# Performance work log

Measured on AMD Instinct MI355X. Metric: run time of the kernel, lower is better.

Reference implementation:

```python
import jax, jax.numpy as jnp
import numpy as np

HEADS = 12
HEAD_SIZE = 64
HIDDEN = 768


def _rope_tables(seqlen, dim, dtype):
    inv_freq = 1.0 / (10000.0 ** (jnp.arange(0, dim, 2, dtype=jnp.float32) / dim))
    t = jnp.arange(seqlen, dtype=jnp.float32)
    freqs = t[:, None] * inv_freq[None, :]  # [L, dim/2]
    return jnp.sin(freqs).astype(dtype), jnp.cos(freqs).astype(dtype)


def _apply_rope(x, sin, cos):
    # x: [B, L, H, D]; sin/cos: [L, D/2] -> broadcast as [1, L, 1, D/2]
    sin = sin[None, :, None, :]
    cos = cos[None, :, None, :]
    x1 = x[..., 0::2]
    x2 = x[..., 1::2]
    out1 = x1 * cos - x2 * sin
    out2 = x1 * sin + x2 * cos
    # interleave back: stack on new last axis then flatten
    return jnp.stack([out1, out2], axis=-1).reshape(x.shape)


def setup_inputs() -> dict:
    key = jax.random.key(0)
    k1, k2, k3 = jax.random.split(key, 3)
    B, L = 8, 512
    inputs = jax.random.normal(k1, (B, L, HIDDEN), dtype=jnp.float32)
    attention_mask = jnp.ones((B, L), dtype=jnp.int32)
    out_dim = HEADS * 2 * HEAD_SIZE
    W = jax.random.normal(k2, (HIDDEN, out_dim), dtype=jnp.float32) * (1.0 / np.sqrt(HIDDEN))
    b = jax.random.normal(k3, (out_dim,), dtype=jnp.float32) * 0.02
    return {"inputs": inputs, "W": W, "b": b, "attention_mask": attention_mask}


def reference(inputs, W, b, attention_mask):
    B, L, _ = inputs.shape
    x = inputs @ W + b  # [B, L, H*2*D]
    x = x.reshape(B, L, HEADS, 2, HEAD_SIZE)
    qw = x[..., 0, :]  # [B, L, H, D]
    kw = x[..., 1, :]
    sin, cos = _rope_tables(L, HEAD_SIZE, x.dtype)
    qw = _apply_rope(qw, sin, cos)
    kw = _apply_rope(kw, sin, cos)
    logits = jnp.einsum('bmhd,bnhd->bhmn', qw, kw) / np.sqrt(HEAD_SIZE)
    neg_inf = jnp.finfo(logits.dtype).min
    am = attention_mask.astype(bool)
    valid = am[:, None, None, :] & am[:, None, :, None]
    logits = jnp.where(valid, logits, neg_inf)
    tri = jnp.tril(jnp.ones((L, L), dtype=bool), k=-1)
    logits = jnp.where(tri[None, None, :, :], neg_inf, logits)
    return logits
```

## Files before the change

### kernel.cpp

```cpp
#include <hip/hip_runtime.h>
#include <hip/hip_bf16.h>
#include <math.h>
#include <stdint.h>

constexpr int BATCH  = 8;
constexpr int SEQ    = 512;
constexpr int HEADS  = 12;
constexpr int HSIZE  = 64;
constexpr int HIDDEN = 768;
constexpr int OUTD   = 1536;
constexpr int M      = BATCH * SEQ;
constexpr int BH     = BATCH * HEADS;

#define NEG_INF (-3.3895313892515355e38f)

typedef short  s16x8 __attribute__((ext_vector_type(8)));
typedef float  f32x4 __attribute__((ext_vector_type(4)));

__device__ __forceinline__ short f2bf(float f) {
    __hip_bfloat16 h = __float2bfloat16(f);
    return *reinterpret_cast<short*>(&h);
}

__device__ __forceinline__ void g2l16(const void* g, void* l) {
    __builtin_amdgcn_global_load_lds(
        reinterpret_cast<const __attribute__((address_space(1))) int*>(
            reinterpret_cast<uintptr_t>(g)),
        reinterpret_cast<__attribute__((address_space(3))) int*>(
            reinterpret_cast<uintptr_t>(l)),
        16, 0, 0);
}

__global__ __launch_bounds__(256) void prep_kernel(
    const float* __restrict__ X,  short* __restrict__ Xb,
    const float* __restrict__ W,  short* __restrict__ Wt,
    float* __restrict__ sc_sin,   float* __restrict__ sc_cos)
{
    __shared__ short Ls[32][36];
    const int b   = blockIdx.x;
    const int tid = threadIdx.x;

    if (b < 1536) {
        const int t = b * 256 + tid;
        const float4 a = ((const float4*)X)[t * 2];
        const float4 c = ((const float4*)X)[t * 2 + 1];
        s16x8 o;
        o[0] = f2bf(a.x); o[1] = f2bf(a.y); o[2] = f2bf(a.z); o[3] = f2bf(a.w);
        o[4] = f2bf(c.x); o[5] = f2bf(c.y); o[6] = f2bf(c.z); o[7] = f2bf(c.w);
        ((s16x8*)Xb)[t] = o;
    } else if (b < 2688) {
        const int bid = b - 1536;
        const int nx = bid % 48, ky = bid / 48;
        const int r  = tid >> 3;
        const int c4 = (tid & 7) * 4;
        const float4 v = *(const float4*)(W + (size_t)(ky * 32 + r) * OUTD + nx * 32 + c4);
        Ls[r][c4 + 0] = f2bf(v.x); Ls[r][c4 + 1] = f2bf(v.y);
        Ls[r][c4 + 2] = f2bf(v.z); Ls[r][c4 + 3] = f2bf(v.w);
        __syncthreads();
        short4 ov;
        ov.x = Ls[c4 + 0][r]; ov.y = Ls[c4 + 1][r];
        ov.z = Ls[c4 + 2][r]; ov.w = Ls[c4 + 3][r];
        *(short4*)(Wt + (size_t)(nx * 32 + r) * HIDDEN + ky * 32 + c4) = ov;
    } else {
        const int t   = (b - 2688) * 256 + tid;
        const int pos = t >> 5, pi = t & 31;
        const float invf = exp2f((float)(2 * pi) * (-13.287712379549449f / 64.0f));
        const float ang  = (float)pos * invf;
        sc_sin[t] = sinf(ang);
        sc_cos[t] = cosf(ang);
    }
}

__global__ __launch_bounds__(256) void proj_mfma_kernel(
    const short* __restrict__ Xb,
    const short* __restrict__ Wt,
    const float* __restrict__ bias,
    const float* __restrict__ sc_sin,
    const float* __restrict__ sc_cos,
    short* __restrict__ Qb,
    short* __restrict__ Kb)
{
    union Sh {
        struct { short As[2][128 * 64]; short Bs[2][64 * 64]; } st;
        float epi[128 * 68];
    };
    __shared__ Sh sh;

    const int tid = threadIdx.x;
    const int l   = tid & 63;
    const int w   = tid >> 6;
    const int mBase = blockIdx.y * 128;
    const int nBase = blockIdx.x * 64;
    const int wm = w * 32;

    const int lr = l >> 3;
    const int gc = (l & 7) ^ lr;
    const short* aSrc = Xb + (size_t)(mBase + wm + lr)     * HIDDEN + gc * 8;
    const short* bSrc = Wt + (size_t)(nBase + w * 16 + lr) * HIDDEN + gc * 8;

#define STAGE(buf_, k0_)                                                     \
    do {                                                                     \
        _Pragma("unroll")                                                    \
        for (int p = 0; p < 4; ++p)                                          \
            g2l16(aSrc + (k0_) + p * 8 * HIDDEN,                             \
                  sh.st.As[buf_] + (w * 4 + p) * 512);                       \
        _Pragma("unroll")                                                    \
        for (int p = 0; p < 2; ++p)                                          \
            g2l16(bSrc + (k0_) + p * 8 * HIDDEN,                             \
                  sh.st.Bs[buf_] + (w * 2 + p) * 512);                       \
    } while (0)

    STAGE(0, 0);
    __syncthreads();

    f32x4 acc[2][4] = {};
    int buf = 0;

    for (int k0 = 0; k0 < HIDDEN; k0 += 64) {
        if (k0 + 64 < HIDDEN)
            STAGE(buf ^ 1, k0 + 64);
        const short* Asb = sh.st.As[buf];
        const short* Bsb = sh.st.Bs[buf];
#pragma unroll
        for (int s = 0; s < 2; ++s) {
            const int c = ((s * 4 + (l >> 4)) ^ (l & 7)) * 8;
            s16x8 af[2], bf[4];
#pragma unroll
            for (int i = 0; i < 2; ++i)
                af[i] = *(const s16x8*)(Asb + (wm + i * 16 + (l & 15)) * 64 + c);
#pragma unroll
            for (int j = 0; j < 4; ++j)
                bf[j] = *(const s16x8*)(Bsb + (j * 16 + (l & 15)) * 64 + c);
#pragma unroll
            for (int i = 0; i < 2; ++i)
#pragma unroll
                for (int j = 0; j < 4; ++j)
                    acc[i][j] = __builtin_amdgcn_mfma_f32_16x16x32_bf16(
                        af[i], bf[j], acc[i][j], 0, 0, 0);
        }
        __syncthreads();
        buf ^= 1;
    }
#undef STAGE

    const int colL = l & 15, quad = l >> 4;
#pragma unroll
    for (int j = 0; j < 4; ++j) {
        const int nl = j * 16 + colL;
#pragma unroll
        for (int i = 0; i < 2; ++i)
#pragma unroll
            for (int r = 0; r < 4; ++r)
                sh.epi[(wm + i * 16 + quad * 4 + r) * 68 + nl] = acc[i][j][r];
    }
    __syncthreads();

    const int bb   = mBase >> 9;
    const int pos0 = mBase & 511;
    const int h    = nBase >> 7;
    const int slot = (nBase >> 6) & 1;
    short* dst = (slot ? Kb : Qb) + ((size_t)(bb * HEADS + h) * SEQ + pos0) * HSIZE;

#pragma unroll
    for (int p = 0; p < 4; ++p) {
        const int c    = tid + p * 256;
        const int mrow = c >> 3;
        const int ch   = c & 7;
        const int dloc = ch * 8;
        const int pos  = pos0 + mrow;

        const float* src = &sh.epi[mrow * 68 + dloc];
        const float4 v0 = *(const float4*)(src);
        const float4 v1 = *(const float4*)(src + 4);
        const float* bp = bias + nBase + dloc;
        const float4 b0 = *(const float4*)(bp);
        const float4 b1 = *(const float4*)(bp + 4);
        const float4 sn = *(const float4*)(sc_sin + pos * 32 + (dloc >> 1));
        const float4 cs = *(const float4*)(sc_cos + pos * 32 + (dloc >> 1));

        const float e0 = v0.x + b0.x, o0 = v0.y + b0.y;
        const float e1 = v0.z + b0.z, o1 = v0.w + b0.w;
        const float e2 = v1.x + b1.x, o2 = v1.y + b1.y;
        const float e3 = v1.z + b1.z, o3 = v1.w + b1.w;
        s16x8 ov;
        ov[0] = f2bf(e0 * cs.x - o0 * sn.x); ov[1] = f2bf(e0 * sn.x + o0 * cs.x);
        ov[2] = f2bf(e1 * cs.y - o1 * sn.y); ov[3] = f2bf(e1 * sn.y + o1 * cs.y);
        ov[4] = f2bf(e2 * cs.z - o2 * sn.z); ov[5] = f2bf(e2 * sn.z + o2 * cs.z);
        ov[6] = f2bf(e3 * cs.w - o3 * sn.w); ov[7] = f2bf(e3 * sn.w + o3 * cs.w);
        *(s16x8*)(dst + (size_t)mrow * HSIZE + dloc) = ov;
    }
}

__global__ __launch_bounds__(256) void qk_mfma_kernel(
    const short* __restrict__ Qb,
    const short* __restrict__ Kb,
    const int*   __restrict__ am,
    float* __restrict__ out)
{
    const int bh = blockIdx.z;
    const int bb = bh / HEADS;
    const int m0 = blockIdx.y * 128;
    const int n0 = blockIdx.x * 128;
    const int tid = threadIdx.x;

    if (m0 >= n0 + 128) {
        const float4 ninf = make_float4(NEG_INF, NEG_INF, NEG_INF, NEG_INF);
        float* base = out + ((size_t)bh * SEQ + m0) * SEQ + n0;
        const int c = (tid & 31) * 4;
#pragma unroll
        for (int r = 0; r < 16; ++r) {
            const int row = r * 8 + (tid >> 5);
            *(float4*)(base + (size_t)row * SEQ + c) = ninf;
        }
        return;
    }

    __shared__ short Qs[128 * 64];
    __shared__ short Ks[128 * 64];
    __shared__ __align__(16) int amR[128];
    __shared__ __align__(16) int amC[128];

    const int l = tid & 63;
    const int w = tid >> 6;
    if (tid < 128)      amR[tid]       = am[bb * SEQ + m0 + tid];
    else                amC[tid - 128] = am[bb * SEQ + n0 + (tid - 128)];

    const int lr = l >> 3;
    const int gc = (l & 7) ^ lr;
    const short* qSrc = Qb + ((size_t)bh * SEQ + m0 + w * 32 + lr) * HSIZE + gc * 8;
    const short* kSrc = Kb + ((size_t)bh * SEQ + n0 + w * 32 + lr) * HSIZE + gc * 8;
#pragma unroll
    for (int p = 0; p < 4; ++p) {
        g2l16(qSrc + p * 8 * HSIZE, Qs + (w * 4 + p) * 512);
        g2l16(kSrc + p * 8 * HSIZE, Ks + (w * 4 + p) * 512);
    }
    __syncthreads();

    const int wm = (w & 1) * 64;
    const int wn = (w >> 1) * 64;
    f32x4 acc[4][4] = {};
#pragma unroll
    for (int s = 0; s < 2; ++s) {
        const int c = ((s * 4 + (l >> 4)) ^ (l & 7)) * 8;
        s16x8 qf[4], kf[4];
#pragma unroll
        for (int i = 0; i < 4; ++i) {
            qf[i] = *(const s16x8*)(Qs + (wm + i * 16 + (l & 15)) * 64 + c);
            kf[i] = *(const s16x8*)(Ks + (wn + i * 16 + (l & 15)) * 64 + c);
        }
#pragma unroll
        for (int i = 0; i < 4; ++i)
#pragma unroll
            for (int j = 0; j < 4; ++j)
                acc[i][j] = __builtin_amdgcn_mfma_f32_16x16x32_bf16(
                    qf[i], kf[j], acc[i][j], 0, 0, 0);
    }

    const int colL = l & 15, quad = l >> 4;
    int rm[4][4];
#pragma unroll
    for (int i = 0; i < 4; ++i)
#pragma unroll
        for (int r = 0; r < 4; ++r)
            rm[i][r] = amR[wm + i * 16 + quad * 4 + r];

#pragma unroll
    for (int j = 0; j < 4; ++j) {
        const int nl = wn + j * 16 + colL;
        const int ng = n0 + nl;
        const int an = amC[nl];
#pragma unroll
        for (int i = 0; i < 4; ++i) {
#pragma unroll
            for (int r = 0; r < 4; ++r) {
                const int ml = wm + i * 16 + quad * 4 + r;
                const int mg = m0 + ml;
                float v = acc[i][j][r] * 0.125f;
                if (ng < mg || !an || !rm[i][r]) v = NEG_INF;
                out[((size_t)bh * SEQ + mg) * SEQ + ng] = v;
            }
        }
    }
}

extern "C" void kernel_launch(void* const* d_in, const int* in_sizes, int n_in,
                              void* d_out, int out_size, void* d_ws, size_t ws_size,
                              hipStream_t stream) {
    const float* X    = (const float*)d_in[0];
    const float* W    = (const float*)d_in[1];
    const float* bias = (const float*)d_in[2];
    const int*   am   = (const int*)d_in[3];
    float* out = (float*)d_out;

    char* ws = (char*)d_ws;
    short* Xb = (short*)(ws);
    short* Wt = (short*)(ws + 6291456);
    short* Qb = (short*)(ws + 8650752);
    short* Kb = (short*)(ws + 14942208);
    float* sc_sin = (float*)(ws + 21233664);
    float* sc_cos = (float*)(ws + 21299200);

    prep_kernel<<<dim3(2752), 256, 0, stream>>>(X, Xb, W, Wt, sc_sin, sc_cos);
    proj_mfma_kernel<<<dim3(OUTD / 64, M / 128), 256, 0, stream>>>(
        Xb, Wt, bias, sc_sin, sc_cos, Qb, Kb);
    qk_mfma_kernel<<<dim3(SEQ / 128, SEQ / 128, BH), 256, 0, stream>>>(Qb, Kb, am, out);
}
```

Baseline: 144.3 us.

## Fuse prep, projection and QK kernels into one cooperative persistent kernel

Merges the three launches into a single cooperative kernel of 768 blocks. Grid-wide syncs separate the bf16 conversion and RoPE table phase, the projection GEMM phase and the QK logits phase. The aim is to remove launch overhead and inter-kernel gaps. In exchange it adds two grid barriers, limits occupancy to a fixed grid (launch_bounds 256,3), and grid-strides the prep and QK phases, so each block does about two QK tiles serially.

```diff
diff --git a/kernel.cpp b/kernel.cpp
--- a/kernel.cpp
+++ b/kernel.cpp
@@ -1,7 +1,10 @@
 #include <hip/hip_runtime.h>
+#include <hip/hip_cooperative_groups.h>
 #include <hip/hip_bf16.h>
 #include <math.h>
 #include <stdint.h>
+
+namespace cg = cooperative_groups;
 
 constexpr int BATCH  = 8;
 constexpr int SEQ    = 512;
@@ -31,253 +34,247 @@
         16, 0, 0);
 }
 
-__global__ __launch_bounds__(256) void prep_kernel(
-    const float* __restrict__ X,  short* __restrict__ Xb,
-    const float* __restrict__ W,  short* __restrict__ Wt,
-    float* __restrict__ sc_sin,   float* __restrict__ sc_cos)
+__global__ __launch_bounds__(256, 3) void fused_kernel(
+    const float* __restrict__ X,      short* __restrict__ Xb,
+    const float* __restrict__ W,      short* __restrict__ Wt,
+    const float* __restrict__ bias,
+    float* __restrict__ sc_sin,       float* __restrict__ sc_cos,
+    short* __restrict__ Qb,           short* __restrict__ Kb,
+    const int* __restrict__ am,       float* __restrict__ out)
 {
-    __shared__ short Ls[32][36];
-    const int b   = blockIdx.x;
-    const int tid = threadIdx.x;
-
-    if (b < 1536) {
-        const int t = b * 256 + tid;
-        const float4 a = ((const float4*)X)[t * 2];
-        const float4 c = ((const float4*)X)[t * 2 + 1];
-        s16x8 o;
-        o[0] = f2bf(a.x); o[1] = f2bf(a.y); o[2] = f2bf(a.z); o[3] = f2bf(a.w);
-        o[4] = f2bf(c.x); o[5] = f2bf(c.y); o[6] = f2bf(c.z); o[7] = f2bf(c.w);
-        ((s16x8*)Xb)[t] = o;
-    } else if (b < 2688) {
-        const int bid = b - 1536;
-        const int nx = bid % 48, ky = bid / 48;
-        const int r  = tid >> 3;
-        const int c4 = (tid & 7) * 4;
-        const float4 v = *(const float4*)(W + (size_t)(ky * 32 + r) * OUTD + nx * 32 + c4);
-        Ls[r][c4 + 0] = f2bf(v.x); Ls[r][c4 + 1] = f2bf(v.y);
-        Ls[r][c4 + 2] = f2bf(v.z); Ls[r][c4 + 3] = f2bf(v.w);
-        __syncthreads();
-        short4 ov;
-        ov.x = Ls[c4 + 0][r]; ov.y = Ls[c4 + 1][r];
-        ov.z = Ls[c4 + 2][r]; ov.w = Ls[c4 + 3][r];
-        *(short4*)(Wt + (size_t)(nx * 32 + r) * HIDDEN + ky * 32 + c4) = ov;
-    } else {
-        const int t   = (b - 2688) * 256 + tid;
-        const int pos = t >> 5, pi = t & 31;
-        const float invf = exp2f((float)(2 * pi) * (-13.287712379549449f / 64.0f));
-        const float ang  = (float)pos * invf;
-        sc_sin[t] = sinf(ang);
-        sc_cos[t] = cosf(ang);
-    }
-}
-
-__global__ __launch_bounds__(256) void proj_mfma_kernel(
-    const short* __restrict__ Xb,
-    const short* __restrict__ Wt,
-    const float* __restrict__ bias,
-    const float* __restrict__ sc_sin,
-    const float* __restrict__ sc_cos,
-    short* __restrict__ Qb,
-    short* __restrict__ Kb)
-{
-    union Sh {
-        struct { short As[2][128 * 64]; short Bs[2][64 * 64]; } st;
-        float epi[128 * 68];
-    };
-    __shared__ Sh sh;
+    __shared__ __align__(16) union {
+        short Ls[32][36];
+        union {
+            struct { short As[2][128 * 64]; short Bs[2][64 * 64]; } st;
+            float epi[128 * 68];
+        } proj;
+        struct { short Qs[128 * 64]; short Ks[128 * 64];
+                 int amR[128]; int amC[128]; } qk;
+    } sh;
 
     const int tid = threadIdx.x;
     const int l   = tid & 63;
     const int w   = tid >> 6;
-    const int mBase = blockIdx.y * 128;
-    const int nBase = blockIdx.x * 64;
-    const int wm = w * 32;
-
-    const int lr = l >> 3;
-    const int gc = (l & 7) ^ lr;
-    const short* aSrc = Xb + (size_t)(mBase + wm + lr)     * HIDDEN + gc * 8;
-    const short* bSrc = Wt + (size_t)(nBase + w * 16 + lr) * HIDDEN + gc * 8;
+
+    for (int vb = blockIdx.x; vb < 2752; vb += 768) {
+        __syncthreads();
+        if (vb < 1536) {
+            const int t = vb * 256 + tid;
+            const float4 a = ((const float4*)X)[t * 2];
+            const float4 c = ((const float4*)X)[t * 2 + 1];
+            s16x8 o;
+            o[0] = f2bf(a.x); o[1] = f2bf(a.y); o[2] = f2bf(a.z); o[3] = f2bf(a.w);
+            o[4] = f2bf(c.x); o[5] = f2bf(c.y); o[6] = f2bf(c.z); o[7] = f2bf(c.w);
+            ((s16x8*)Xb)[t] = o;
+        } else if (vb < 2688) {
+            const int bid = vb - 1536;
+            const int nx = bid % 48, ky = bid / 48;
+            const int r  = tid >> 3;
+            const int c4 = (tid & 7) * 4;
+            const float4 v = *(const float4*)(W + (size_t)(ky * 32 + r) * OUTD + nx * 32 + c4);
+            sh.Ls[r][c4 + 0] = f2bf(v.x); sh.Ls[r][c4 + 1] = f2bf(v.y);
+            sh.Ls[r][c4 + 2] = f2bf(v.z); sh.Ls[r][c4 + 3] = f2bf(v.w);
+            __syncthreads();
+            short4 ov;
+            ov.x = sh.Ls[c4 + 0][r]; ov.y = sh.Ls[c4 + 1][r];
+            ov.z = sh.Ls[c4 + 2][r]; ov.w = sh.Ls[c4 + 3][r];
+            *(short4*)(Wt + (size_t)(nx * 32 + r) * HIDDEN + ky * 32 + c4) = ov;
+        } else {
+            const int t   = (vb - 2688) * 256 + tid;
+            const int pos = t >> 5, pi = t & 31;
+            const float invf = exp2f((float)(2 * pi) * (-13.287712379549449f / 64.0f));
+            const float ang  = (float)pos * invf;
+            sc_sin[t] = sinf(ang);
+            sc_cos[t] = cosf(ang);
+        }
+    }
+
+    __threadfence();
+    cg::this_grid().sync();
+
+    {
+        const int mBase = (blockIdx.x / 24) * 128;
+        const int nBase = (blockIdx.x % 24) * 64;
+        const int wm = w * 32;
+
+        const int lr = l >> 3;
+        const int gc = (l & 7) ^ lr;
+        const short* aSrc = Xb + (size_t)(mBase + wm + lr)     * HIDDEN + gc * 8;
+        const short* bSrc = Wt + (size_t)(nBase + w * 16 + lr) * HIDDEN + gc * 8;
 
 #define STAGE(buf_, k0_)                                                     \
     do {                                                                     \
         _Pragma("unroll")                                                    \
         for (int p = 0; p < 4; ++p)                                          \
             g2l16(aSrc + (k0_) + p * 8 * HIDDEN,                             \
-                  sh.st.As[buf_] + (w * 4 + p) * 512);                       \
+                  sh.proj.st.As[buf_] + (w * 4 + p) * 512);                  \
         _Pragma("unroll")                                                    \
         for (int p = 0; p < 2; ++p)                                          \
             g2l16(bSrc + (k0_) + p * 8 * HIDDEN,                             \
-                  sh.st.Bs[buf_] + (w * 2 + p) * 512);                       \
+                  sh.proj.st.Bs[buf_] + (w * 2 + p) * 512);                  \
     } while (0)
 
-    STAGE(0, 0);
-    __syncthreads();
-
-    f32x4 acc[2][4] = {};
-    int buf = 0;
-
-    for (int k0 = 0; k0 < HIDDEN; k0 += 64) {
-        if (k0 + 64 < HIDDEN)
-            STAGE(buf ^ 1, k0 + 64);
-        const short* Asb = sh.st.As[buf];
-        const short* Bsb = sh.st.Bs[buf];
+        STAGE(0, 0);
+        __syncthreads();
+
+        f32x4 acc[2][4] = {};
+        int buf = 0;
+
+        for (int k0 = 0; k0 < HIDDEN; k0 += 64) {
+            if (k0 + 64 < HIDDEN)
+                STAGE(buf ^ 1, k0 + 64);
+            const short* Asb = sh.proj.st.As[buf];
+            const short* Bsb = sh.proj.st.Bs[buf];
+#pragma unroll
+            for (int s = 0; s < 2; ++s) {
+                const int c = ((s * 4 + (l >> 4)) ^ (l & 7)) * 8;
+                s16x8 af[2], bf[4];
+#pragma unroll
+                for (int i = 0; i < 2; ++i)
+                    af[i] = *(const s16x8*)(Asb + (wm + i * 16 + (l & 15)) * 64 + c);
+#pragma unroll
+                for (int j = 0; j < 4; ++j)
+                    bf[j] = *(const s16x8*)(Bsb + (j * 16 + (l & 15)) * 64 + c);
+#pragma unroll
+                for (int i = 0; i < 2; ++i)
+#pragma unroll
+                    for (int j = 0; j < 4; ++j)
+                        acc[i][j] = __builtin_amdgcn_mfma_f32_16x16x32_bf16(
+                            af[i], bf[j], acc[i][j], 0, 0, 0);
+            }
+            __syncthreads();
+            buf ^= 1;
+        }
+#undef STAGE
+
+        const int colL = l & 15, quad = l >> 4;
+#pragma unroll
+        for (int j = 0; j < 4; ++j) {
+            const int nl = j * 16 + colL;
+#pragma unroll
+            for (int i = 0; i < 2; ++i)
+#pragma unroll
+                for (int r = 0; r < 4; ++r)
+                    sh.proj.epi[(wm + i * 16 + quad * 4 + r) * 68 + nl] = acc[i][j][r];
+        }
+        __syncthreads();
+
+        const int bb   = mBase >> 9;
+        const int pos0 = mBase & 511;
+        const int h    = nBase >> 7;
+        const int slot = (nBase >> 6) & 1;
+        short* dst = (slot ? Kb : Qb) + ((size_t)(bb * HEADS + h) * SEQ + pos0) * HSIZE;
+
+#pragma unroll
+        for (int p = 0; p < 4; ++p) {
+            const int c    = tid + p * 256;
+            const int mrow = c >> 3;
+            const int ch   = c & 7;
+            const int dloc = ch * 8;
+            const int pos  = pos0 + mrow;
+
+            const float* src = &sh.proj.epi[mrow * 68 + dloc];
+            const float4 v0 = *(const float4*)(src);
+            const float4 v1 = *(const float4*)(src + 4);
+            const float* bp = bias + nBase + dloc;
+            const float4 b0 = *(const float4*)(bp);
+            const float4 b1 = *(const float4*)(bp + 4);
+            const float4 sn = *(const float4*)(sc_sin + pos * 32 + (dloc >> 1));
+            const float4 cs = *(const float4*)(sc_cos + pos * 32 + (dloc >> 1));
+
+            const float e0 = v0.x + b0.x, o0 = v0.y + b0.y;
+            const float e1 = v0.z + b0.z, o1 = v0.w + b0.w;
+            const float e2 = v1.x + b1.x, o2 = v1.y + b1.y;
+            const float e3 = v1.z + b1.z, o3 = v1.w + b1.w;
+            s16x8 ov;
+            ov[0] = f2bf(e0 * cs.x - o0 * sn.x); ov[1] = f2bf(e0 * sn.x + o0 * cs.x);
+            ov[2] = f2bf(e1 * cs.y - o1 * sn.y); ov[3] = f2bf(e1 * sn.y + o1 * cs.y);
+            ov[4] = f2bf(e2 * cs.z - o2 * sn.z); ov[5] = f2bf(e2 * sn.z + o2 * cs.z);
+            ov[6] = f2bf(e3 * cs.w - o3 * sn.w); ov[7] = f2bf(e3 * sn.w + o3 * cs.w);
+            *(s16x8*)(dst + (size_t)mrow * HSIZE + dloc) = ov;
+        }
+    }
+
+    __threadfence();
+    cg::this_grid().sync();
+
+    for (int t = blockIdx.x; t < 1536; t += 768) {
+        const int n0  = (t & 3) * 128;
+        const int m0  = ((t >> 2) & 3) * 128;
+        const int bh  = t >> 4;
+        const int bb  = bh / HEADS;
+
+        __syncthreads();
+
+        if (m0 >= n0 + 128) {
+            const float4 ninf = make_float4(NEG_INF, NEG_INF, NEG_INF, NEG_INF);
+            float* base = out + ((size_t)bh * SEQ + m0) * SEQ + n0;
+            const int c = (tid & 31) * 4;
+#pragma unroll
+            for (int r = 0; r < 16; ++r) {
+                const int row = r * 8 + (tid >> 5);
+                *(float4*)(base + (size_t)row * SEQ + c) = ninf;
+            }
+            continue;
+        }
+
+        if (tid < 128)      sh.qk.amR[tid]       = am[bb * SEQ + m0 + tid];
+        else                sh.qk.amC[tid - 128] = am[bb * SEQ + n0 + (tid - 128)];
+
+        const int lr = l >> 3;
+        const int gc = (l & 7) ^ lr;
+        const short* qSrc = Qb + ((size_t)bh * SEQ + m0 + w * 32 + lr) * HSIZE + gc * 8;
+        const short* kSrc = Kb + ((size_t)bh * SEQ + n0 + w * 32 + lr) * HSIZE + gc * 8;
+#pragma unroll
+        for (int p = 0; p < 4; ++p) {
+            g2l16(qSrc + p * 8 * HSIZE, sh.qk.Qs + (w * 4 + p) * 512);
+            g2l16(kSrc + p * 8 * HSIZE, sh.qk.Ks + (w * 4 + p) * 512);
+        }
+        __syncthreads();
+
+        const int wm = (w & 1) * 64;
+        const int wn = (w >> 1) * 64;
+        f32x4 acc[4][4] = {};
 #pragma unroll
         for (int s = 0; s < 2; ++s) {
             const int c = ((s * 4 + (l >> 4)) ^ (l & 7)) * 8;
-            s16x8 af[2], bf[4];
-#pragma unroll
-            for (int i = 0; i < 2; ++i)
-                af[i] = *(const s16x8*)(Asb + (wm + i * 16 + (l & 15)) * 64 + c);
-#pragma unroll
-            for (int j = 0; j < 4; ++j)
-                bf[j] = *(const s16x8*)(Bsb + (j * 16 + (l & 15)) * 64 + c);
-#pragma unroll
-            for (int i = 0; i < 2; ++i)
+            s16x8 qf[4], kf[4];
+#pragma unroll
+            for (int i = 0; i < 4; ++i) {
+                qf[i] = *(const s16x8*)(sh.qk.Qs + (wm + i * 16 + (l & 15)) * 64 + c);
+                kf[i] = *(const s16x8*)(sh.qk.Ks + (wn + i * 16 + (l & 15)) * 64 + c);
+            }
+#pragma unroll
+            for (int i = 0; i < 4; ++i)
 #pragma unroll
                 for (int j = 0; j < 4; ++j)
                     acc[i][j] = __builtin_amdgcn_mfma_f32_16x16x32_bf16(
-                        af[i], bf[j], acc[i][j], 0, 0, 0);
-        }
-        __syncthreads();
-        buf ^= 1;
-    }
-#undef STAGE
-
-    const int colL = l & 15, quad = l >> 4;
-#pragma unroll
-    for (int j = 0; j < 4; ++j) {
-        const int nl = j * 16 + colL;
-#pragma unroll
-        for (int i = 0; i < 2; ++i)
+                        qf[i], kf[j], acc[i][j], 0, 0, 0);
+        }
+
+        const int colL = l & 15, quad = l >> 4;
+        int rm[4][4];
+#pragma unroll
+        for (int i = 0; i < 4; ++i)
 #pragma unroll
             for (int r = 0; r < 4; ++r)
-                sh.epi[(wm + i * 16 + quad * 4 + r) * 68 + nl] = acc[i][j][r];
-    }
-    __syncthreads();
-
-    const int bb   = mBase >> 9;
-    const int pos0 = mBase & 511;
-    const int h    = nBase >> 7;
-    const int slot = (nBase >> 6) & 1;
-    short* dst = (slot ? Kb : Qb) + ((size_t)(bb * HEADS + h) * SEQ + pos0) * HSIZE;
-
-#pragma unroll
-    for (int p = 0; p < 4; ++p) {
-        const int c    = tid + p * 256;
-        const int mrow = c >> 3;
-        const int ch   = c & 7;
-        const int dloc = ch * 8;
-        const int pos  = pos0 + mrow;
-
-        const float* src = &sh.epi[mrow * 68 + dloc];
-        const float4 v0 = *(const float4*)(src);
-        const float4 v1 = *(const float4*)(src + 4);
-        const float* bp = bias + nBase + dloc;
-        const float4 b0 = *(const float4*)(bp);
-        const float4 b1 = *(const float4*)(bp + 4);
-        const float4 sn = *(const float4*)(sc_sin + pos * 32 + (dloc >> 1));
-        const float4 cs = *(const float4*)(sc_cos + pos * 32 + (dloc >> 1));
-
-        const float e0 = v0.x + b0.x, o0 = v0.y + b0.y;
-        const float e1 = v0.z + b0.z, o1 = v0.w + b0.w;
-        const float e2 = v1.x + b1.x, o2 = v1.y + b1.y;
-        const float e3 = v1.z + b1.z, o3 = v1.w + b1.w;
-        s16x8 ov;
-        ov[0] = f2bf(e0 * cs.x - o0 * sn.x); ov[1] = f2bf(e0 * sn.x + o0 * cs.x);
-        ov[2] = f2bf(e1 * cs.y - o1 * sn.y); ov[3] = f2bf(e1 * sn.y + o1 * cs.y);
-        ov[4] = f2bf(e2 * cs.z - o2 * sn.z); ov[5] = f2bf(e2 * sn.z + o2 * cs.z);
-        ov[6] = f2bf(e3 * cs.w - o3 * sn.w); ov[7] = f2bf(e3 * sn.w + o3 * cs.w);
-        *(s16x8*)(dst + (size_t)mrow * HSIZE + dloc) = ov;
-    }
-}
-
-__global__ __launch_bounds__(256) void qk_mfma_kernel(
-    const short* __restrict__ Qb,
-    const short* __restrict__ Kb,
-    const int*   __restrict__ am,
-    float* __restrict__ out)
-{
-    const int bh = blockIdx.z;
-    const int bb = bh / HEADS;
-    const int m0 = blockIdx.y * 128;
-    const int n0 = blockIdx.x * 128;
-    const int tid = threadIdx.x;
-
-    if (m0 >= n0 + 128) {
-        const float4 ninf = make_float4(NEG_INF, NEG_INF, NEG_INF, NEG_INF);
-        float* base = out + ((size_t)bh * SEQ + m0) * SEQ + n0;
-        const int c = (tid & 31) * 4;
-#pragma unroll
-        for (int r = 0; r < 16; ++r) {
-            const int row = r * 8 + (tid >> 5);
-            *(float4*)(base + (size_t)row * SEQ + c) = ninf;
-        }
-        return;
-    }
-
-    __shared__ short Qs[128 * 64];
-    __shared__ short Ks[128 * 64];
-    __shared__ __align__(16) int amR[128];
-    __shared__ __align__(16) int amC[128];
-
-    const int l = tid & 63;
-    const int w = tid >> 6;
-    if (tid < 128)      amR[tid]       = am[bb * SEQ + m0 + tid];
-    else                amC[tid - 128] = am[bb * SEQ + n0 + (tid - 128)];
-
-    const int lr = l >> 3;
-    const int gc = (l & 7) ^ lr;
-    const short* qSrc = Qb + ((size_t)bh * SEQ + m0 + w * 32 + lr) * HSIZE + gc * 8;
-    const short* kSrc = Kb + ((size_t)bh * SEQ + n0 + w * 32 + lr) * HSIZE + gc * 8;
-#pragma unroll
-    for (int p = 0; p < 4; ++p) {
-        g2l16(qSrc + p * 8 * HSIZE, Qs + (w * 4 + p) * 512);
-        g2l16(kSrc + p * 8 * HSIZE, Ks + (w * 4 + p) * 512);
-    }
-    __syncthreads();
-
-    const int wm = (w & 1) * 64;
-    const int wn = (w >> 1) * 64;
-    f32x4 acc[4][4] = {};
-#pragma unroll
-    for (int s = 0; s < 2; ++s) {
-        const int c = ((s * 4 + (l >> 4)) ^ (l & 7)) * 8;
-        s16x8 qf[4], kf[4];
-#pragma unroll
-        for (int i = 0; i < 4; ++i) {
-            qf[i] = *(const s16x8*)(Qs + (wm + i * 16 + (l & 15)) * 64 + c);
-            kf[i] = *(const s16x8*)(Ks + (wn + i * 16 + (l & 15)) * 64 + c);
-        }
-#pragma unroll
-        for (int i = 0; i < 4; ++i)
-#pragma unroll
-            for (int j = 0; j < 4; ++j)
-                acc[i][j] = __builtin_amdgcn_mfma_f32_16x16x32_bf16(
-                    qf[i], kf[j], acc[i][j], 0, 0, 0);
-    }
-
-    const int colL = l & 15, quad = l >> 4;
-    int rm[4][4];
-#pragma unroll
-    for (int i = 0; i < 4; ++i)
-#pragma unroll
-        for (int r = 0; r < 4; ++r)
-            rm[i][r] = amR[wm + i * 16 + quad * 4 + r];
-
-#pragma unroll
-    for (int j = 0; j < 4; ++j) {
-        const int nl = wn + j * 16 + colL;
-        const int ng = n0 + nl;
-        const int an = amC[nl];
-#pragma unroll
-        for (int i = 0; i < 4; ++i) {
-#pragma unroll
-            for (int r = 0; r < 4; ++r) {
-                const int ml = wm + i * 16 + quad * 4 + r;
-                const int mg = m0 + ml;
-                float v = acc[i][j][r] * 0.125f;
-                if (ng < mg || !an || !rm[i][r]) v = NEG_INF;
-                out[((size_t)bh * SEQ + mg) * SEQ + ng] = v;
+                rm[i][r] = sh.qk.amR[wm + i * 16 + quad * 4 + r];
+
+#pragma unroll
+        for (int j = 0; j < 4; ++j) {
+            const int nl = wn + j * 16 + colL;
+            const int ng = n0 + nl;
+            const int an = sh.qk.amC[nl];
+#pragma unroll
+            for (int i = 0; i < 4; ++i) {
+#pragma unroll
+                for (int r = 0; r < 4; ++r) {
+                    const int ml = wm + i * 16 + quad * 4 + r;
+                    const int mg = m0 + ml;
+                    float v = acc[i][j][r] * 0.125f;
+                    if (ng < mg || !an || !rm[i][r]) v = NEG_INF;
+                    out[((size_t)bh * SEQ + mg) * SEQ + ng] = v;
+                }
             }
         }
     }
@@ -300,8 +297,9 @@
     float* sc_sin = (float*)(ws + 21233664);
     float* sc_cos = (float*)(ws + 21299200);
 
-    prep_kernel<<<dim3(2752), 256, 0, stream>>>(X, Xb, W, Wt, sc_sin, sc_cos);
-    proj_mfma_kernel<<<dim3(OUTD / 64, M / 128), 256, 0, stream>>>(
-        Xb, Wt, bias, sc_sin, sc_cos, Qb, Kb);
-    qk_mfma_kernel<<<dim3(SEQ / 128, SEQ / 128, BH), 256, 0, stream>>>(Qb, Kb, am, out);
+    void* args[] = { (void*)&X, (void*)&Xb, (void*)&W, (void*)&Wt, (void*)&bias,
+                     (void*)&sc_sin, (void*)&sc_cos, (void*)&Qb, (void*)&Kb,
+                     (void*)&am, (void*)&out };
+    hipLaunchCooperativeKernel((const void*)fused_kernel, dim3(768), dim3(256),
+                               args, 0, stream);
 }
```

New measurement: 466.1 us. 223% more time.
